# Kernel optimization log

Hardware: AMD Instinct MI355X
Metric: run time of the kernel (lower is better)

## Reference

```python
import jax, jax.numpy as jnp
import numpy as np

EPS = 1e-5

def _layer_norm(y, w, b):
    mu = y.mean(-1, keepdims=True)
    var = jnp.mean((y - mu) ** 2, axis=-1, keepdims=True)
    return (y - mu) * jax.lax.rsqrt(var + EPS) * w + b


def setup_inputs() -> dict:
    key = jax.random.key(0)
    ks = jax.random.split(key, 8)
    B, D, H, W = 1, 96, 96, 96
    N, R, K = 16, 6, 4
    x = jax.random.normal(ks[0], (B, D, H, W), jnp.float32)
    x_proj_weight = jax.random.normal(ks[1], (K, R + 2 * N, D), jnp.float32) * 0.05
    dt_projs_weight = jax.random.normal(ks[2], (K, D, R), jnp.float32) * 0.1
    dt_projs_bias = jax.random.normal(ks[3], (K, D), jnp.float32) * 0.1
    A_logs = jax.random.normal(ks[4], (K * D, N), jnp.float32)
    Ds = jax.random.normal(ks[5], (K * D,), jnp.float32) * 0.1
    ln_w = jnp.ones((D,), jnp.float32)
    ln_b = jnp.zeros((D,), jnp.float32)
    return {"x": x, "x_proj_weight": x_proj_weight, "dt_projs_weight": dt_projs_weight,
            "dt_projs_bias": dt_projs_bias, "A_logs": A_logs, "Ds": Ds,
            "ln_w": ln_w, "ln_b": ln_b}


def reference(x, x_proj_weight, dt_projs_weight, dt_projs_bias, A_logs, Ds, ln_w, ln_b):
    B, D, H, W = x.shape
    L = H * W
    K = x_proj_weight.shape[0]            # 4 scan directions
    N = A_logs.shape[1]                   # d_state
    R = dt_projs_weight.shape[2]          # dt_rank

    # ---- CrossScan: 4 directional flattenings -> xs [B, K, D, L]
    xs0 = x.reshape(B, D, L)
    xs1 = jnp.swapaxes(x, 2, 3).reshape(B, D, L)
    xs = jnp.stack([xs0, xs1, xs0[:, :, ::-1], xs1[:, :, ::-1]], axis=1)

    # ---- input-dependent projections
    x_dbl = jnp.einsum('bkdl,kcd->bkcl', xs, x_proj_weight)    # [B,K,R+2N,L]
    dts = x_dbl[:, :, :R]
    Bs = x_dbl[:, :, R:R + N]                                  # [B,K,N,L]
    Cs = x_dbl[:, :, R + N:]                                   # [B,K,N,L]
    dts = jnp.einsum('bkrl,kdr->bkdl', dts, dt_projs_weight)   # [B,K,D,L]

    # ---- selective scan (S6), delta_softplus=True, fp32
    delta = jax.nn.softplus(dts + dt_projs_bias[None, :, :, None])   # [B,K,D,L]
    A = -jnp.exp(A_logs).reshape(K, D, N)                             # [K,D,N]
    dA = jnp.exp(jnp.einsum('bkdl,kdn->bkdln', delta, A))             # [B,K,D,L,N]
    dBu = jnp.einsum('bkdl,bknl,bkdl->bkdln', delta, Bs, xs)          # delta*B*u

    def combine(c1, c2):
        a1, b1 = c1
        a2, b2 = c2
        return a1 * a2, a2 * b1 + b2

    _, h = jax.lax.associative_scan(combine, (dA, dBu), axis=3)       # h_t over L

    y = jnp.einsum('bkdln,bknl->bkdl', h, Cs)
    y = y + xs * Ds.reshape(K, D)[None, :, :, None]                   # [B,K,D,L]

    # ---- CrossMerge: undo the 4 directional scans and sum
    ys = y[:, 0:2] + y[:, 2:4, :, ::-1]                               # [B,2,D,L]
    ym = ys[:, 0] + jnp.swapaxes(ys[:, 1].reshape(B, D, W, H), 2, 3).reshape(B, D, L)

    # ---- out_norm (LayerNorm over D) and reshape to [B,H,W,D]
    yout = jnp.swapaxes(ym, 1, 2)                                     # [B,L,D]
    yout = _layer_norm(yout, ln_w, ln_b).reshape(B, H, W, D)
    return yout.astype(x.dtype)
```

## Files before the change

### kernel.cpp

```cpp
#include <hip/hip_runtime.h>
#include <math.h>

constexpr int cD = 96, cL = 9216, cK = 4;
constexpr int CL = 72, NCH = 128;
constexpr float LOG2E = 1.44269504088896f;

constexpr long OFF_XT    = 0;
constexpr long OFF_DELTA = OFF_XT    + (long)cD*cL;
constexpr long OFF_BS    = OFF_DELTA + 4L*cD*cL;
constexpr long OFF_CS    = OFF_BS    + 4L*cL*16;
constexpr long OFF_Y     = OFF_CS    + 4L*cL*16;

__device__ __forceinline__ float4 a2prep(float4 v) {
    return make_float4(-LOG2E * exp2f(LOG2E * v.x), -LOG2E * exp2f(LOG2E * v.y),
                       -LOG2E * exp2f(LOG2E * v.z), -LOG2E * exp2f(LOG2E * v.w));
}

__global__ __launch_bounds__(256) void kT(const float* __restrict__ x,
                                          float* __restrict__ xT) {
    __shared__ float t[32][33];
    const int h0 = blockIdx.x * 32, w0 = blockIdx.y * 32, d = blockIdx.z;
    const float* xd = x + (long)d * cL;
    float* xtd = xT + (long)d * cL;
    for (int o = threadIdx.x; o < 1024; o += 256) {
        int i = o >> 5, j = o & 31;
        t[i][j] = xd[(h0 + i) * 96 + w0 + j];
    }
    __syncthreads();
    for (int o = threadIdx.x; o < 1024; o += 256) {
        int i = o >> 5, j = o & 31;
        xtd[(w0 + i) * 96 + h0 + j] = t[j][i];
    }
}

__global__ __launch_bounds__(256) void kA(const float* __restrict__ x,
                                          const float* __restrict__ xT,
                                          const float* __restrict__ xpw,
                                          const float* __restrict__ dtw,
                                          const float* __restrict__ dtb,
                                          float* __restrict__ delta,
                                          float* __restrict__ Bs,
                                          float* __restrict__ Cs) {
    __shared__ float xs[96][64];
    __shared__ float xdbl[38][65];
    __shared__ float dtw_l[96 * 6];
    __shared__ float dtb_l[96];
    const int p0 = blockIdx.x * 64;
    const int k  = blockIdx.y;
    const int tid = threadIdx.x;
    const float* src = (k & 1) ? xT : x;

    for (int o = tid; o < 96 * 64; o += 256) {
        int dd = o >> 6, pp = o & 63;
        xs[dd][pp] = src[(long)dd * cL + p0 + pp];
    }
    for (int o = tid; o < 96 * 6; o += 256) dtw_l[o] = dtw[k * 96 * 6 + o];
    if (tid < 96) dtb_l[tid] = dtb[k * 96 + tid];
    __syncthreads();

    const int lane = tid & 63;
    const int c0 = __builtin_amdgcn_readfirstlane((tid >> 6) * 10);
    const float* wk = xpw + (long)k * 38 * 96;
    float acc[10];
    #pragma unroll
    for (int i = 0; i < 10; ++i) acc[i] = 0.f;
    #pragma unroll 4
    for (int dd = 0; dd < 96; ++dd) {
        float xv = xs[dd][lane];
        #pragma unroll
        for (int i = 0; i < 10; ++i) {
            int c = c0 + i; c = c > 37 ? 37 : c;
            acc[i] = fmaf(xv, wk[c * 96 + dd], acc[i]);
        }
    }
    #pragma unroll
    for (int i = 0; i < 10; ++i) {
        int c = c0 + i; c = c > 37 ? 37 : c;
        xdbl[c][lane] = acc[i];
    }
    __syncthreads();

    for (int o = tid; o < 64 * 16; o += 256) {
        int n = o & 15, pp = o >> 4;
        int P = p0 + pp;
        int q = (k < 2) ? P : (9215 - P);
        int ch = q / 72, j = q - ch * 72;
        long idx = (((long)k * 72 + j) * 128 + ch) * 16 + n;
        Bs[idx] = xdbl[6 + n][pp];
        Cs[idx] = xdbl[22 + n][pp];
    }
    for (int o = tid; o < 96 * 64; o += 256) {
        int dd = o >> 6, pp = o & 63;
        float s = dtb_l[dd];
        #pragma unroll
        for (int r = 0; r < 6; ++r) s = fmaf(xdbl[r][pp], dtw_l[dd * 6 + r], s);
        float sp = fmaxf(s, 0.f) + __logf(1.f + __expf(-fabsf(s)));
        delta[((long)(k * 96 + dd)) * cL + p0 + pp] = sp;
    }
}

__global__ __launch_bounds__(512, 4) void kS(const float* __restrict__ x,
                                             const float* __restrict__ xT,
                                             const float* __restrict__ delta,
                                             const float* __restrict__ Bs,
                                             const float* __restrict__ Cs,
                                             const float* __restrict__ Alog,
                                             const float* __restrict__ Dsv,
                                             float* __restrict__ y) {
    __shared__ float lp[NCH][16];
    __shared__ float ls[NCH][16];
    __shared__ float ybuf[9216 + 96];
    float* gpf = &lp[0][0];
    const int tid = threadIdx.x;
    const int seq = blockIdx.x;
    const int k = seq / 96, d = seq % 96, rev = k >> 1;
    const int n0 = (tid & 3) * 4, ch = tid >> 2;
    const int q0 = rev ? (9215 - ch * CL) : ch * CL;

    const float4 a2 = a2prep(*(const float4*)(Alog + (long)seq * 16 + n0));
    const float Dv = Dsv[seq];
    const float* dB = delta + (long)seq * cL + q0;
    const float* xB = ((k & 1) ? xT : x) + (long)d * cL + q0;
    const float* bB = Bs + (long)k * cL * 16 + (long)ch * 16 + n0;
    const float* cB = Cs + (long)k * cL * 16 + (long)ch * 16 + n0;

    float4 h = make_float4(0.f, 0.f, 0.f, 0.f);
    float sdl = 0.f;
#define S1(DL, XV, OFF) { \
        float4 B = *(const float4*)(bB + (OFF) * 2048); \
        float t = (DL) * (XV); sdl += (DL); \
        h.x = fmaf(exp2f((DL)*a2.x), h.x, t*B.x); \
        h.y = fmaf(exp2f((DL)*a2.y), h.y, t*B.y); \
        h.z = fmaf(exp2f((DL)*a2.z), h.z, t*B.z); \
        h.w = fmaf(exp2f((DL)*a2.w), h.w, t*B.w); }
    if (!rev) {
        #pragma unroll
        for (int g = 0; g < 18; ++g) {
            float4 d4 = *(const float4*)(dB + 4*g);
            float4 x4 = *(const float4*)(xB + 4*g);
            S1(d4.x, x4.x, 4*g)   S1(d4.y, x4.y, 4*g+1)
            S1(d4.z, x4.z, 4*g+2) S1(d4.w, x4.w, 4*g+3)
        }
    } else {
        #pragma unroll
        for (int g = 0; g < 18; ++g) {
            float4 d4 = *(const float4*)(dB - 4*g - 3);
            float4 x4 = *(const float4*)(xB - 4*g - 3);
            S1(d4.w, x4.w, 4*g)   S1(d4.z, x4.z, 4*g+1)
            S1(d4.y, x4.y, 4*g+2) S1(d4.x, x4.x, 4*g+3)
        }
    }
#undef S1
    *(float4*)&lp[ch][n0] = make_float4(exp2f(a2.x*sdl), exp2f(a2.y*sdl),
                                        exp2f(a2.z*sdl), exp2f(a2.w*sdl));
    *(float4*)&ls[ch][n0] = h;
    __syncthreads();

    const int sn = tid & 15, sg = tid >> 4;
    float LPe[4], LSe[4];
    {
        float P = 1.f, S = 0.f;
        #pragma unroll
        for (int i = 0; i < 4; ++i) {
            LPe[i] = P; LSe[i] = S;
            float p = lp[sg * 4 + i][sn], s = ls[sg * 4 + i][sn];
            S = fmaf(p, S, s); P = p * P;
        }
        __syncthreads();
        gpf[tid] = P; gpf[512 + tid] = S;
    }
    __syncthreads();
    #pragma unroll
    for (int off = 1; off < 32; off <<= 1) {
        float pc = gpf[tid], sc = gpf[512 + tid];
        float pn = pc, snn = sc;
        if (sg >= off) {
            pn  = pc * gpf[tid - off * 16];
            snn = fmaf(pc, gpf[512 + tid - off * 16], sc);
        }
        __syncthreads();
        gpf[tid] = pn; gpf[512 + tid] = snn;
        __syncthreads();
    }
    const float GS = (sg == 0) ? 0.f : gpf[512 + tid - 16];
    #pragma unroll
    for (int i = 0; i < 4; ++i) ls[sg * 4 + i][sn] = fmaf(LPe[i], GS, LSe[i]);
    __syncthreads();

    h = *(float4*)&ls[ch][n0];
    const int slB = ch * CL;
    const bool lane0 = (tid & 3) == 0;
#define S2(DL, XV, OFF) { \
        float4 B = *(const float4*)(bB + (OFF) * 2048); \
        float4 C = *(const float4*)(cB + (OFF) * 2048); \
        float t = (DL) * (XV); \
        h.x = fmaf(exp2f((DL)*a2.x), h.x, t*B.x); \
        h.y = fmaf(exp2f((DL)*a2.y), h.y, t*B.y); \
        h.z = fmaf(exp2f((DL)*a2.z), h.z, t*B.z); \
        h.w = fmaf(exp2f((DL)*a2.w), h.w, t*B.w); \
        float pv = fmaf(h.x, C.x, fmaf(h.y, C.y, fmaf(h.z, C.z, h.w * C.w))); \
        pv += __shfl_xor(pv, 1, 4); \
        pv += __shfl_xor(pv, 2, 4); \
        if (lane0) { int sl = slB + (OFF); int yloc = rev ? 9215 - sl : sl; \
                     ybuf[yloc + yloc / 96] = fmaf(Dv, (XV), pv); } }
    if (!rev) {
        #pragma unroll
        for (int g = 0; g < 18; ++g) {
            float4 d4 = *(const float4*)(dB + 4*g);
            float4 x4 = *(const float4*)(xB + 4*g);
            S2(d4.x, x4.x, 4*g)   S2(d4.y, x4.y, 4*g+1)
            S2(d4.z, x4.z, 4*g+2) S2(d4.w, x4.w, 4*g+3)
        }
    } else {
        #pragma unroll
        for (int g = 0; g < 18; ++g) {
            float4 d4 = *(const float4*)(dB - 4*g - 3);
            float4 x4 = *(const float4*)(xB - 4*g - 3);
            S2(d4.w, x4.w, 4*g)   S2(d4.z, x4.z, 4*g+1)
            S2(d4.y, x4.y, 4*g+2) S2(d4.x, x4.x, 4*g+3)
        }
    }
#undef S2
    __syncthreads();

    float* yrow = y + (long)seq * cL;
    if (k & 1) {
        for (int o = tid; o < 9216; o += 512) {
            int hh = o / 96, wl = o - hh * 96;
            yrow[o] = ybuf[wl * 97 + hh];
        }
    } else {
        for (int o = tid; o < 9216; o += 512) {
            yrow[o] = ybuf[o + o / 96];
        }
    }
}

__global__ __launch_bounds__(256) void kE(const float* __restrict__ y,
                                          const float* __restrict__ lnw,
                                          const float* __restrict__ lnb,
                                          float* __restrict__ out) {
    __shared__ float vs[96][36];
    __shared__ float red[8][32], red2[8][32];
    __shared__ float MU[32], RS[32];
    const int tid = threadIdx.x;
    const int p0 = blockIdx.x * 32;

    for (int o = tid; o < 96 * 8; o += 256) {
        int dd = o >> 3, j = o & 7;
        const float* r0 = y + (long)dd * cL + p0;
        const float* r1 = y + (long)(96 + dd) * cL + p0;
        const float* r2 = y + (long)(192 + dd) * cL + p0;
        const float* r3 = y + (long)(288 + dd) * cL + p0;
        float4 a = ((const float4*)r0)[j];
        float4 b = ((const float4*)r1)[j];
        float4 c = ((const float4*)r2)[j];
        float4 e = ((const float4*)r3)[j];
        *(float4*)&vs[dd][4 * j] = make_float4(a.x + b.x + c.x + e.x,
                                               a.y + b.y + c.y + e.y,
                                               a.z + b.z + c.z + e.z,
                                               a.w + b.w + c.w + e.w);
    }
    __syncthreads();

    const int p = tid & 31, part = tid >> 5;
    float s = 0.f, s2 = 0.f;
    for (int dd = part * 12; dd < part * 12 + 12; ++dd) {
        float v = vs[dd][p];
        s += v; s2 = fmaf(v, v, s2);
    }
    red[part][p] = s; red2[part][p] = s2;
    __syncthreads();
    if (tid < 32) {
        float S = 0.f, S2 = 0.f;
        #pragma unroll
        for (int q = 0; q < 8; ++q) { S += red[q][tid]; S2 += red2[q][tid]; }
        float m = S * (1.f / 96.f);
        MU[tid] = m;
        RS[tid] = rsqrtf(S2 * (1.f / 96.f) - m * m + 1e-5f);
    }
    __syncthreads();
    for (int o = tid; o < 32 * 96; o += 256) {
        int pl = o / 96, dd = o - pl * 96;
        out[(long)(p0 + pl) * 96 + dd] = (vs[dd][pl] - MU[pl]) * RS[pl] * lnw[dd] + lnb[dd];
    }
}

extern "C" void kernel_launch(void* const* d_in, const int* in_sizes, int n_in,
                              void* d_out, int out_size, void* d_ws, size_t ws_size,
                              hipStream_t stream) {
    const float* x    = (const float*)d_in[0];
    const float* xpw  = (const float*)d_in[1];
    const float* dtw  = (const float*)d_in[2];
    const float* dtb  = (const float*)d_in[3];
    const float* Alog = (const float*)d_in[4];
    const float* Dsv  = (const float*)d_in[5];
    const float* lnw  = (const float*)d_in[6];
    const float* lnb  = (const float*)d_in[7];
    float* ws = (float*)d_ws;

    float* xT    = ws + OFF_XT;
    float* delta = ws + OFF_DELTA;
    float* Bs    = ws + OFF_BS;
    float* Cs    = ws + OFF_CS;
    float* y     = ws + OFF_Y;
    float* out   = (float*)d_out;

    kT<<<dim3(3, 3, 96), 256, 0, stream>>>(x, xT);
    kA<<<dim3(144, 4), 256, 0, stream>>>(x, xT, xpw, dtw, dtb, delta, Bs, Cs);
    kS<<<cK * cD, 512, 0, stream>>>(x, xT, delta, Bs, Cs, Alog, Dsv, y);
    kE<<<288, 256, 0, stream>>>(y, lnw, lnb, out);
}
```

Measured before the change: 104.6 us.

## Write scan outputs directly from registers and move transpose into separate kernel

The scan kernel drops its ~37KB shared-memory y buffer and its end-of-kernel permuted copy. Each quad instead holds its reduced output in a register and writes a float4-strided group straight to global memory, in scan order. The quad reduction now uses DPP moves instead of shuffles. Reversal is undone inside the LayerNorm kernel, and the transpose for directions 1 and 3 is done by a new transpose kernel into an extra workspace buffer. This frees LDS for occupancy in the scan kernel, at the cost of an extra kernel launch and an extra pass over half of y.

After: 99.54 us. 4.9% less time.

```diff
diff --git a/kernel.cpp b/kernel.cpp
--- a/kernel.cpp
+++ b/kernel.cpp
@@ -3,17 +3,23 @@
 
 constexpr int cD = 96, cL = 9216, cK = 4;
 constexpr int CL = 72, NCH = 128;
+constexpr long cDL = (long)cD * cL;
 constexpr float LOG2E = 1.44269504088896f;
 
 constexpr long OFF_XT    = 0;
-constexpr long OFF_DELTA = OFF_XT    + (long)cD*cL;
-constexpr long OFF_BS    = OFF_DELTA + 4L*cD*cL;
+constexpr long OFF_DELTA = OFF_XT    + cDL;
+constexpr long OFF_BS    = OFF_DELTA + 4L*cDL;
 constexpr long OFF_CS    = OFF_BS    + 4L*cL*16;
 constexpr long OFF_Y     = OFF_CS    + 4L*cL*16;
+constexpr long OFF_YT    = OFF_Y     + 4L*cDL;
 
 __device__ __forceinline__ float4 a2prep(float4 v) {
     return make_float4(-LOG2E * exp2f(LOG2E * v.x), -LOG2E * exp2f(LOG2E * v.y),
                        -LOG2E * exp2f(LOG2E * v.z), -LOG2E * exp2f(LOG2E * v.w));
+}
+template<int C>
+__device__ __forceinline__ float qperm(float v) {
+    return __int_as_float(__builtin_amdgcn_mov_dpp(__float_as_int(v), C, 0xf, 0xf, true));
 }
 
 __global__ __launch_bounds__(256) void kT(const float* __restrict__ x,
@@ -109,12 +115,12 @@
                                              float* __restrict__ y) {
     __shared__ float lp[NCH][16];
     __shared__ float ls[NCH][16];
-    __shared__ float ybuf[9216 + 96];
     float* gpf = &lp[0][0];
     const int tid = threadIdx.x;
     const int seq = blockIdx.x;
     const int k = seq / 96, d = seq % 96, rev = k >> 1;
     const int n0 = (tid & 3) * 4, ch = tid >> 2;
+    const int r = tid & 3;
     const int q0 = rev ? (9215 - ch * CL) : ch * CL;
 
     const float4 a2 = a2prep(*(const float4*)(Alog + (long)seq * 16 + n0));
@@ -188,9 +194,9 @@
     __syncthreads();
 
     h = *(float4*)&ls[ch][n0];
-    const int slB = ch * CL;
-    const bool lane0 = (tid & 3) == 0;
-#define S2(DL, XV, OFF) { \
+    float* yq = y + (long)seq * cL + ch * CL;
+    float yhold = 0.f;
+#define S2(DL, XV, SI, OFF) { \
         float4 B = *(const float4*)(bB + (OFF) * 2048); \
         float4 C = *(const float4*)(cB + (OFF) * 2048); \
         float t = (DL) * (XV); \
@@ -199,44 +205,52 @@
         h.z = fmaf(exp2f((DL)*a2.z), h.z, t*B.z); \
         h.w = fmaf(exp2f((DL)*a2.w), h.w, t*B.w); \
         float pv = fmaf(h.x, C.x, fmaf(h.y, C.y, fmaf(h.z, C.z, h.w * C.w))); \
-        pv += __shfl_xor(pv, 1, 4); \
-        pv += __shfl_xor(pv, 2, 4); \
-        if (lane0) { int sl = slB + (OFF); int yloc = rev ? 9215 - sl : sl; \
-                     ybuf[yloc + yloc / 96] = fmaf(Dv, (XV), pv); } }
+        pv += qperm<0xB1>(pv); \
+        pv += qperm<0x4E>(pv); \
+        if ((SI) == r) yhold = fmaf(Dv, (XV), pv); }
     if (!rev) {
         #pragma unroll
         for (int g = 0; g < 18; ++g) {
             float4 d4 = *(const float4*)(dB + 4*g);
             float4 x4 = *(const float4*)(xB + 4*g);
-            S2(d4.x, x4.x, 4*g)   S2(d4.y, x4.y, 4*g+1)
-            S2(d4.z, x4.z, 4*g+2) S2(d4.w, x4.w, 4*g+3)
+            S2(d4.x, x4.x, 0, 4*g)   S2(d4.y, x4.y, 1, 4*g+1)
+            S2(d4.z, x4.z, 2, 4*g+2) S2(d4.w, x4.w, 3, 4*g+3)
+            yq[4*g + r] = yhold;
         }
     } else {
         #pragma unroll
         for (int g = 0; g < 18; ++g) {
             float4 d4 = *(const float4*)(dB - 4*g - 3);
             float4 x4 = *(const float4*)(xB - 4*g - 3);
-            S2(d4.w, x4.w, 4*g)   S2(d4.z, x4.z, 4*g+1)
-            S2(d4.y, x4.y, 4*g+2) S2(d4.x, x4.x, 4*g+3)
+            S2(d4.w, x4.w, 0, 4*g)   S2(d4.z, x4.z, 1, 4*g+1)
+            S2(d4.y, x4.y, 2, 4*g+2) S2(d4.x, x4.x, 3, 4*g+3)
+            yq[4*g + r] = yhold;
         }
     }
 #undef S2
-    __syncthreads();
-
-    float* yrow = y + (long)seq * cL;
-    if (k & 1) {
-        for (int o = tid; o < 9216; o += 512) {
-            int hh = o / 96, wl = o - hh * 96;
-            yrow[o] = ybuf[wl * 97 + hh];
-        }
-    } else {
-        for (int o = tid; o < 9216; o += 512) {
-            yrow[o] = ybuf[o + o / 96];
-        }
-    }
-}
-
-__global__ __launch_bounds__(256) void kE(const float* __restrict__ y,
+}
+
+__global__ __launch_bounds__(256) void kU(const float* __restrict__ Y,
+                                          float* __restrict__ YT) {
+    __shared__ float t[32][33];
+    const int i0 = blockIdx.x * 32, j0 = blockIdx.y * 32;
+    const int z = blockIdx.z;
+    const int arr = z / 96, d = z % 96;
+    const float* src = Y + (1 + 2 * arr) * cDL + (long)d * cL;
+    float* dst = YT + (long)arr * cDL + (long)d * cL;
+    for (int o = threadIdx.x; o < 1024; o += 256) {
+        int i = o >> 5, j = o & 31;
+        t[i][j] = src[(i0 + i) * 96 + j0 + j];
+    }
+    __syncthreads();
+    for (int o = threadIdx.x; o < 1024; o += 256) {
+        int i = o >> 5, j = o & 31;
+        dst[(j0 + i) * 96 + i0 + j] = t[j][i];
+    }
+}
+
+__global__ __launch_bounds__(256) void kE(const float* __restrict__ Y,
+                                          const float* __restrict__ YT,
                                           const float* __restrict__ lnw,
                                           const float* __restrict__ lnb,
                                           float* __restrict__ out) {
@@ -248,18 +262,18 @@
 
     for (int o = tid; o < 96 * 8; o += 256) {
         int dd = o >> 3, j = o & 7;
-        const float* r0 = y + (long)dd * cL + p0;
-        const float* r1 = y + (long)(96 + dd) * cL + p0;
-        const float* r2 = y + (long)(192 + dd) * cL + p0;
-        const float* r3 = y + (long)(288 + dd) * cL + p0;
+        const float* r0 = Y + (long)dd * cL + p0;
+        const float* r1 = YT + (long)dd * cL + p0;
+        const float* r2 = Y + 2 * cDL + (long)dd * cL;
+        const float* r3 = YT + cDL + (long)dd * cL;
         float4 a = ((const float4*)r0)[j];
         float4 b = ((const float4*)r1)[j];
-        float4 c = ((const float4*)r2)[j];
-        float4 e = ((const float4*)r3)[j];
-        *(float4*)&vs[dd][4 * j] = make_float4(a.x + b.x + c.x + e.x,
-                                               a.y + b.y + c.y + e.y,
-                                               a.z + b.z + c.z + e.z,
-                                               a.w + b.w + c.w + e.w);
+        float4 c = *(const float4*)(r2 + 9212 - p0 - 4 * j);
+        float4 e = *(const float4*)(r3 + 9212 - p0 - 4 * j);
+        *(float4*)&vs[dd][4 * j] = make_float4(a.x + b.x + c.w + e.w,
+                                               a.y + b.y + c.z + e.z,
+                                               a.z + b.z + c.y + e.y,
+                                               a.w + b.w + c.x + e.x);
     }
     __syncthreads();
 
@@ -304,10 +318,12 @@
     float* Bs    = ws + OFF_BS;
     float* Cs    = ws + OFF_CS;
     float* y     = ws + OFF_Y;
+    float* yT    = ws + OFF_YT;
     float* out   = (float*)d_out;
 
     kT<<<dim3(3, 3, 96), 256, 0, stream>>>(x, xT);
     kA<<<dim3(144, 4), 256, 0, stream>>>(x, xT, xpw, dtw, dtb, delta, Bs, Cs);
     kS<<<cK * cD, 512, 0, stream>>>(x, xT, delta, Bs, Cs, Alog, Dsv, y);
-    kE<<<288, 256, 0, stream>>>(y, lnw, lnb, out);
-}
+    kU<<<dim3(3, 3, 192), 256, 0, stream>>>(y, yT);
+    kE<<<288, 256, 0, stream>>>(y, yT, lnw, lnb, out);
+}
```
